# Optimization experiments

Hardware: AMD Instinct MI355X
Metric: run time of the kernel (lower is better)

The kernel has to match this reference:

```python
import jax, jax.numpy as jnp
import numpy as np

D_MODEL = 1024
N_HEADS = 16


def setup_inputs() -> dict:
    key0 = jax.random.key(0)
    ks = jax.random.split(key0, 13)
    B, Lq, Lk, D = 2, 1024, 2048, D_MODEL
    scale = 0.02
    inp = {
        "query": jax.random.normal(ks[0], (B, Lq, D), jnp.float32),
        "key": jax.random.normal(ks[1], (B, Lk, D), jnp.float32),
        "value": jax.random.normal(ks[2], (B, Lk, D), jnp.float32),
        "mask": jax.random.randint(ks[3], (B, 1, Lq, Lk), 0, 2, jnp.int32),
        "attn_bias": jax.random.normal(ks[4], (B, N_HEADS, Lq, Lk), jnp.float32) * 0.1,
        "Wq": jax.random.normal(ks[5], (D, D), jnp.float32) * scale,
        "bq": jnp.zeros((D,), jnp.float32),
        "Wk": jax.random.normal(ks[6], (D, D), jnp.float32) * scale,
        "bk": jnp.zeros((D,), jnp.float32),
        "Wv": jax.random.normal(ks[7], (D, D), jnp.float32) * scale,
        "bv": jnp.zeros((D,), jnp.float32),
        "Wo": jax.random.normal(ks[8], (D, D), jnp.float32) * scale,
        "bo": jnp.zeros((D,), jnp.float32),
    }
    return inp


def reference(query, key, value, mask, attn_bias, Wq, bq, Wk, bk, Wv, bv, Wo, bo):
    B, Lq, D = query.shape
    Lk = key.shape[1]
    H = N_HEADS
    dh = D // H
    # projections (torch Linear: x @ W.T + b), then split heads -> [B,H,L,dh]
    Q = (query @ Wq.T + bq).reshape(B, Lq, H, dh).transpose(0, 2, 1, 3)
    K = (key @ Wk.T + bk).reshape(B, Lk, H, dh).transpose(0, 2, 1, 3)
    V = (value @ Wv.T + bv).reshape(B, Lk, H, dh).transpose(0, 2, 1, 3)
    scores = jnp.einsum("bhqd,bhkd->bhqk", Q, K) / jnp.sqrt(jnp.float32(dh))
    scores = scores + attn_bias
    scores = jnp.where(mask == 0, jnp.float32(-1e9), scores)
    attn = jax.nn.softmax(scores, axis=-1)  # dropout disabled (eval / p=0)
    out = jnp.einsum("bhqk,bhkd->bhqd", attn, V)
    out = out.transpose(0, 2, 1, 3).reshape(B, Lq, D)
    out = out @ Wo.T + bo
    return out, attn
```

## Files before the change

kernel.cpp:

```cpp
#include <hip/hip_runtime.h>
#include <hip/hip_bf16.h>

typedef __hip_bfloat16 bf16;
typedef __bf16  bf16x8 __attribute__((ext_vector_type(8)));
typedef float   f32x4  __attribute__((ext_vector_type(4)));

static constexpr int DMODEL = 1024;
static constexpr int NHEADS = 16;
static constexpr int DHEAD  = 64;
static constexpr int BATCH  = 2;
static constexpr int SLQ    = 1024;
static constexpr int SLK    = 2048;
static constexpr size_t OUTQ = (size_t)BATCH * SLQ * DMODEL;

__global__ __launch_bounds__(256)
void k_cvt(const float* __restrict__ q,  const float* __restrict__ k,
           const float* __restrict__ v,  const float* __restrict__ wq,
           const float* __restrict__ wk, const float* __restrict__ wv,
           const float* __restrict__ wo,
           bf16* __restrict__ qb,  bf16* __restrict__ kb,  bf16* __restrict__ vb,
           bf16* __restrict__ wqb, bf16* __restrict__ wkb, bf16* __restrict__ wvb,
           bf16* __restrict__ wob)
{
    const int seg = blockIdx.y;
    const float* s; bf16* d; int n;
    switch (seg) {
        case 0:  s = q;  d = qb;  n = 2 * 1024 * 1024; break;
        case 1:  s = k;  d = kb;  n = 4 * 1024 * 1024; break;
        case 2:  s = v;  d = vb;  n = 4 * 1024 * 1024; break;
        case 3:  s = wq; d = wqb; n = 1024 * 1024; break;
        case 4:  s = wk; d = wkb; n = 1024 * 1024; break;
        case 5:  s = wv; d = wvb; n = 1024 * 1024; break;
        default: s = wo; d = wob; n = 1024 * 1024; break;
    }
    const int stride = gridDim.x * blockDim.x;
    for (int i = blockIdx.x * blockDim.x + threadIdx.x; i * 8 < n; i += stride) {
        const float4 a = *(const float4*)(s + (size_t)i * 8);
        const float4 b = *(const float4*)(s + (size_t)i * 8 + 4);
        bf16 h[8] = {__float2bfloat16(a.x), __float2bfloat16(a.y),
                     __float2bfloat16(a.z), __float2bfloat16(a.w),
                     __float2bfloat16(b.x), __float2bfloat16(b.y),
                     __float2bfloat16(b.z), __float2bfloat16(b.w)};
        *(int4*)(d + (size_t)i * 8) = *(const int4*)h;
    }
}

__device__ __forceinline__ void gemm128(const bf16* __restrict__ A,
                                        const bf16* __restrict__ W,
                                        int m0, int n0, f32x4 acc[4][4])
{
    __shared__ __align__(16) unsigned short As[128][40];
    __shared__ __align__(16) unsigned short Bs[128][40];
    const int tid  = threadIdx.x;
    const int lane = tid & 63, w = tid >> 6;
    const int wr = (w >> 1) * 64, wc = (w & 1) * 64;
    const int lr = lane & 15, lk = lane >> 4;
    const int srow = tid >> 1;
    const int scol = (tid & 1) * 16;

    const bf16* Ap = A + (size_t)(m0 + srow) * DMODEL + scol;
    const bf16* Wp = W + (size_t)(n0 + srow) * DMODEL + scol;

    for (int kt = 0; kt < DMODEL; kt += 32) {
        *(int4*)&As[srow][scol]     = *(const int4*)(Ap + kt);
        *(int4*)&As[srow][scol + 8] = *(const int4*)(Ap + kt + 8);
        *(int4*)&Bs[srow][scol]     = *(const int4*)(Wp + kt);
        *(int4*)&Bs[srow][scol + 8] = *(const int4*)(Wp + kt + 8);
        __syncthreads();
        bf16x8 av[4], wv[4];
#pragma unroll
        for (int i = 0; i < 4; ++i)
            av[i] = *(const bf16x8*)&As[wr + i * 16 + lr][lk * 8];
#pragma unroll
        for (int j = 0; j < 4; ++j)
            wv[j] = *(const bf16x8*)&Bs[wc + j * 16 + lr][lk * 8];
#pragma unroll
        for (int i = 0; i < 4; ++i)
#pragma unroll
            for (int j = 0; j < 4; ++j)
                acc[i][j] = __builtin_amdgcn_mfma_f32_16x16x32_bf16(av[i], wv[j], acc[i][j], 0, 0, 0);
        __syncthreads();
    }
}

__global__ __launch_bounds__(256)
void k_qkv(const bf16* __restrict__ qb, const bf16* __restrict__ kb,
           const bf16* __restrict__ vb2,
           const bf16* __restrict__ wqb, const bf16* __restrict__ wkb,
           const bf16* __restrict__ wvb,
           const float* __restrict__ bq, const float* __restrict__ bk,
           const float* __restrict__ bvv,
           bf16* __restrict__ Qp, bf16* __restrict__ Kp, bf16* __restrict__ Vt)
{
    const int which = blockIdx.z;
    const int m0 = blockIdx.x * 128, n0 = blockIdx.y * 128;
    if (which == 0 && m0 >= BATCH * SLQ) return;
    const bf16* A = which == 0 ? qb : which == 1 ? kb : vb2;
    const bf16* W = which == 0 ? wqb : which == 1 ? wkb : wvb;
    const float* bias = which == 0 ? bq : which == 1 ? bk : bvv;

    f32x4 acc[4][4] = {};
    gemm128(A, W, m0, n0, acc);

    const int tid = threadIdx.x, lane = tid & 63, w = tid >> 6;
    const int wr = (w >> 1) * 64, wc = (w & 1) * 64;
    const int lr = lane & 15, lk = lane >> 4;

    if (which < 2) {
        bf16* C = which == 0 ? Qp : Kp;
#pragma unroll
        for (int i = 0; i < 4; ++i)
#pragma unroll
            for (int j = 0; j < 4; ++j) {
                const int col = n0 + wc + j * 16 + lr;
                const float bvx = bias[col];
#pragma unroll
                for (int r = 0; r < 4; ++r) {
                    const int row = m0 + wr + i * 16 + lk * 4 + r;
                    C[(size_t)row * DMODEL + col] = __float2bfloat16(acc[i][j][r] + bvx);
                }
            }
    } else {
#pragma unroll
        for (int i = 0; i < 4; ++i)
#pragma unroll
            for (int j = 0; j < 4; ++j) {
                const int col = n0 + wc + j * 16 + lr;
                const float bvx = bias[col];
                const int h = col >> 6, d = col & 63;
                const int mb = m0 + wr + i * 16 + lk * 4;
                const int b = mb >> 11, kk = mb & 2047;
                bf16* dst = Vt + ((size_t)(b * NHEADS + h) * DHEAD + d) * SLK + kk;
#pragma unroll
                for (int r = 0; r < 4; ++r)
                    dst[r] = __float2bfloat16(acc[i][j][r] + bvx);
            }
    }
}

__global__ __launch_bounds__(256)
void k_projO(const bf16* __restrict__ ctx, const bf16* __restrict__ wob,
             const float* __restrict__ bo, float* __restrict__ out)
{
    const int m0 = blockIdx.x * 128, n0 = blockIdx.y * 128;
    f32x4 acc[4][4] = {};
    gemm128(ctx, wob, m0, n0, acc);
    const int tid = threadIdx.x, lane = tid & 63, w = tid >> 6;
    const int wr = (w >> 1) * 64, wc = (w & 1) * 64;
    const int lr = lane & 15, lk = lane >> 4;
#pragma unroll
    for (int i = 0; i < 4; ++i)
#pragma unroll
        for (int j = 0; j < 4; ++j) {
            const int col = n0 + wc + j * 16 + lr;
            const float bvx = bo[col];
#pragma unroll
            for (int r = 0; r < 4; ++r) {
                const int row = m0 + wr + i * 16 + lk * 4 + r;
                out[(size_t)row * DMODEL + col] = acc[i][j][r] + bvx;
            }
        }
}

__global__ __launch_bounds__(1024, 4)
void k_attn(const bf16* __restrict__ Qp, const bf16* __restrict__ Kp,
            const float* __restrict__ bias, const int* __restrict__ mask,
            const bf16* __restrict__ Vt, float* __restrict__ attn,
            bf16* __restrict__ ctx)
{
    constexpr int SST = 2052;
    constexpr int PST = 520;

    __shared__ __align__(16) float S[16 * SST];
    __shared__ __align__(16) bf16  Pc[16 * PST];
    __shared__ float m_s[16], inv_s[16];

    const int qt = blockIdx.x, bh = blockIdx.y;
    const int b = bh >> 4, h = bh & 15;
    const int q0 = qt * 16;
    const int tid  = threadIdx.x;
    const int lane = tid & 63, w = tid >> 6;
    const int lr = lane & 15, lk = lane >> 4;

    const bf16* qb = Qp + ((size_t)(b * SLQ + q0 + lr)) * DMODEL + h * DHEAD + lk * 8;
    const bf16x8 a0 = *(const bf16x8*)qb;
    const bf16x8 a1 = *(const bf16x8*)(qb + 32);

    const bf16* kb = Kp + (size_t)b * SLK * DMODEL + h * DHEAD + lk * 8;
#pragma unroll 2
    for (int ct = 0; ct < 8; ++ct) {
        const int c0 = w * 128 + ct * 16;
        const bf16* kp = kb + (size_t)(c0 + lr) * DMODEL;
        bf16x8 b0 = *(const bf16x8*)kp;
        bf16x8 b1 = *(const bf16x8*)(kp + 32);
        f32x4 acc = {0.f, 0.f, 0.f, 0.f};
        acc = __builtin_amdgcn_mfma_f32_16x16x32_bf16(a0, b0, acc, 0, 0, 0);
        acc = __builtin_amdgcn_mfma_f32_16x16x32_bf16(a1, b1, acc, 0, 0, 0);
#pragma unroll
        for (int r = 0; r < 4; ++r)
            S[(lk * 4 + r) * SST + c0 + lr] = acc[r] * 0.125f;
    }
    __syncthreads();

    {
        float* sp = &S[w * SST];
        const size_t brow = ((size_t)bh * SLQ + q0 + w) * SLK;
        const size_t mrow = ((size_t)b  * SLQ + q0 + w) * SLK;
        float mx = -3.0e38f;
#pragma unroll 2
        for (int j = 0; j < 8; ++j) {
            const int col = j * 256 + lane * 4;
            f32x4 v = *(const f32x4*)(sp + col);
            const float4 bb = *(const float4*)(bias + brow + col);
            const int4  mm = *(const int4*)(mask + mrow + col);
            float s0 = (mm.x == 0) ? -1e9f : v[0] + bb.x;
            float s1 = (mm.y == 0) ? -1e9f : v[1] + bb.y;
            float s2 = (mm.z == 0) ? -1e9f : v[2] + bb.z;
            float s3 = (mm.w == 0) ? -1e9f : v[3] + bb.w;
            f32x4 wv = {s0, s1, s2, s3};
            *(f32x4*)(sp + col) = wv;
            mx = fmaxf(mx, fmaxf(fmaxf(s0, s1), fmaxf(s2, s3)));
        }
#pragma unroll
        for (int d = 1; d < 64; d <<= 1) mx = fmaxf(mx, __shfl_xor(mx, d));
        float l = 0.f;
#pragma unroll 2
        for (int j = 0; j < 8; ++j) {
            const int col = j * 256 + lane * 4;
            const f32x4 v = *(const f32x4*)(sp + col);
            l += __expf(v[0] - mx) + __expf(v[1] - mx)
               + __expf(v[2] - mx) + __expf(v[3] - mx);
        }
#pragma unroll
        for (int d = 1; d < 64; d <<= 1) l += __shfl_xor(l, d);
        if (lane == 0) { m_s[w] = mx; inv_s[w] = 1.0f / l; }
    }
    __syncthreads();

    f32x4 pv = {0.f, 0.f, 0.f, 0.f};
    const int g = w >> 2, dg = w & 3;
    const bf16* vb = Vt + (size_t)bh * DHEAD * SLK + (size_t)(dg * 16 + lr) * SLK + lk * 8;
    for (int c = 0; c < 4; ++c) {
        const int ck0 = c * 512;
        {
            const int scol = lane * 8;
            const float m = m_s[w], inv = inv_s[w];
            const f32x4 s0 = *(const f32x4*)&S[w * SST + ck0 + scol];
            const f32x4 s1 = *(const f32x4*)&S[w * SST + ck0 + scol + 4];
            const f32x4 p0 = {__expf(s0[0] - m) * inv, __expf(s0[1] - m) * inv,
                              __expf(s0[2] - m) * inv, __expf(s0[3] - m) * inv};
            const f32x4 p1 = {__expf(s1[0] - m) * inv, __expf(s1[1] - m) * inv,
                              __expf(s1[2] - m) * inv, __expf(s1[3] - m) * inv};
            float* ap = attn + ((size_t)bh * SLQ + q0 + w) * SLK + ck0 + scol;
            __builtin_nontemporal_store(p0, (f32x4*)ap);
            __builtin_nontemporal_store(p1, (f32x4*)(ap + 4));
            bf16 t8[8] = {__float2bfloat16(p0[0]), __float2bfloat16(p0[1]),
                          __float2bfloat16(p0[2]), __float2bfloat16(p0[3]),
                          __float2bfloat16(p1[0]), __float2bfloat16(p1[1]),
                          __float2bfloat16(p1[2]), __float2bfloat16(p1[3])};
            *(int4*)&Pc[w * PST + scol] = *(const int4*)t8;
        }
        __syncthreads();
        const bf16* vc = vb + ck0;
#pragma unroll
        for (int i = 0; i < 4; ++i) {
            const int koff = (g * 4 + i) * 32;
            bf16x8 pa = *(const bf16x8*)&Pc[lr * PST + koff + lk * 8];
            bf16x8 vv = *(const bf16x8*)(vc + koff);
            pv = __builtin_amdgcn_mfma_f32_16x16x32_bf16(pa, vv, pv, 0, 0, 0);
        }
        __syncthreads();
    }

    float* rbuf = S;
    *(f32x4*)&rbuf[(w * 64 + lane) * 4] = pv;
    __syncthreads();
    if (g == 0) {
        f32x4 t = {0.f, 0.f, 0.f, 0.f};
#pragma unroll
        for (int gg = 0; gg < 4; ++gg)
            t += *(const f32x4*)&rbuf[((gg * 4 + dg) * 64 + lane) * 4];
        const int d = dg * 16 + lr;
#pragma unroll
        for (int r = 0; r < 4; ++r) {
            const int q = lk * 4 + r;
            ctx[((size_t)(b * SLQ + q0 + q)) * DMODEL + h * DHEAD + d] =
                __float2bfloat16(t[r]);
        }
    }
}

extern "C" void kernel_launch(void* const* d_in, const int* in_sizes, int n_in,
                              void* d_out, int out_size, void* d_ws, size_t ws_size,
                              hipStream_t stream)
{
    const float* query = (const float*)d_in[0];
    const float* key   = (const float*)d_in[1];
    const float* value = (const float*)d_in[2];
    const int*   mask  = (const int*)d_in[3];
    const float* bias  = (const float*)d_in[4];
    const float* Wq = (const float*)d_in[5];
    const float* bq = (const float*)d_in[6];
    const float* Wk = (const float*)d_in[7];
    const float* bk = (const float*)d_in[8];
    const float* Wv = (const float*)d_in[9];
    const float* bv = (const float*)d_in[10];
    const float* Wo = (const float*)d_in[11];
    const float* bo = (const float*)d_in[12];

    float* out  = (float*)d_out;
    float* attn = out + OUTQ;

    bf16* Qp  = (bf16*)d_ws;
    bf16* ctx = Qp;
    bf16* Wob = Qp + (size_t)2 * 1024 * 1024;
    bf16* Vt  = Qp + (size_t)4 * 1024 * 1024;
    bf16* Kp  = (bf16*)d_out;

    bf16* qbf = (bf16*)attn;
    bf16* kbf = qbf + (size_t)2 * 1024 * 1024;
    bf16* vbf = kbf + (size_t)4 * 1024 * 1024;
    bf16* Wqb = vbf + (size_t)4 * 1024 * 1024;
    bf16* Wkb = Wqb + (size_t)1024 * 1024;
    bf16* Wvb = Wkb + (size_t)1024 * 1024;

    k_cvt<<<dim3(256, 7), dim3(256), 0, stream>>>(query, key, value, Wq, Wk, Wv, Wo,
                                                  qbf, kbf, vbf, Wqb, Wkb, Wvb, Wob);
    k_qkv<<<dim3(32, 8, 3), dim3(256), 0, stream>>>(qbf, kbf, vbf, Wqb, Wkb, Wvb,
                                                    bq, bk, bv, Qp, Kp, Vt);
    k_attn<<<dim3(SLQ / 16, BATCH * NHEADS), dim3(1024), 0, stream>>>(Qp, Kp, bias, mask, Vt, attn, ctx);
    k_projO<<<dim3(16, 8), dim3(256), 0, stream>>>(ctx, Wob, bo, out);
}
```

Measured before the change: 708.2 us.

## Use direct global-to-LDS loads in GEMM and prefetch bias/mask in attention

The GEMM tile loader now uses global_load_lds, moving data straight from global memory into unpadded LDS tiles instead of staging it through registers. Separately, the attention kernel issues its bias and mask loads for the first 16 rows at kernel start, before the QK^T MFMA, so their latency overlaps the score computation. The unpadded LDS layout (row stride 32) can cause bank conflicts on the MFMA fragment reads. The prefetch holds 64 extra VGPRs per thread, which may lower occupancy.

```diff
diff --git a/kernel.cpp b/kernel.cpp
--- a/kernel.cpp
+++ b/kernel.cpp
@@ -12,6 +12,10 @@
 static constexpr int SLQ    = 1024;
 static constexpr int SLK    = 2048;
 static constexpr size_t OUTQ = (size_t)BATCH * SLQ * DMODEL;
+
+#define GLOAD16(g, l) __builtin_amdgcn_global_load_lds(                        \
+    (const __attribute__((address_space(1))) unsigned int*)(g),                \
+    (__attribute__((address_space(3))) unsigned int*)(l), 16, 0, 0)
 
 __global__ __launch_bounds__(256)
 void k_cvt(const float* __restrict__ q,  const float* __restrict__ k,
@@ -49,31 +53,39 @@
                                         const bf16* __restrict__ W,
                                         int m0, int n0, f32x4 acc[4][4])
 {
-    __shared__ __align__(16) unsigned short As[128][40];
-    __shared__ __align__(16) unsigned short Bs[128][40];
+    __shared__ __align__(16) unsigned short As[128 * 32];
+    __shared__ __align__(16) unsigned short Bs[128 * 32];
     const int tid  = threadIdx.x;
     const int lane = tid & 63, w = tid >> 6;
     const int wr = (w >> 1) * 64, wc = (w & 1) * 64;
     const int lr = lane & 15, lk = lane >> 4;
-    const int srow = tid >> 1;
-    const int scol = (tid & 1) * 16;
-
-    const bf16* Ap = A + (size_t)(m0 + srow) * DMODEL + scol;
-    const bf16* Wp = W + (size_t)(n0 + srow) * DMODEL + scol;
+
+    const int seg0 = w * 2, seg1 = w * 2 + 1;
+    const int r0 = seg0 * 16 + (lane >> 2);
+    const int r1 = seg1 * 16 + (lane >> 2);
+    const int ce = (lane & 3) * 8;
+    const bf16* a0p = A + (size_t)(m0 + r0) * DMODEL + ce;
+    const bf16* a1p = A + (size_t)(m0 + r1) * DMODEL + ce;
+    const bf16* w0p = W + (size_t)(n0 + r0) * DMODEL + ce;
+    const bf16* w1p = W + (size_t)(n0 + r1) * DMODEL + ce;
+    unsigned short* as0 = &As[seg0 * 512];
+    unsigned short* as1 = &As[seg1 * 512];
+    unsigned short* bs0 = &Bs[seg0 * 512];
+    unsigned short* bs1 = &Bs[seg1 * 512];
 
     for (int kt = 0; kt < DMODEL; kt += 32) {
-        *(int4*)&As[srow][scol]     = *(const int4*)(Ap + kt);
-        *(int4*)&As[srow][scol + 8] = *(const int4*)(Ap + kt + 8);
-        *(int4*)&Bs[srow][scol]     = *(const int4*)(Wp + kt);
-        *(int4*)&Bs[srow][scol + 8] = *(const int4*)(Wp + kt + 8);
+        GLOAD16(a0p + kt, as0);
+        GLOAD16(a1p + kt, as1);
+        GLOAD16(w0p + kt, bs0);
+        GLOAD16(w1p + kt, bs1);
         __syncthreads();
         bf16x8 av[4], wv[4];
 #pragma unroll
         for (int i = 0; i < 4; ++i)
-            av[i] = *(const bf16x8*)&As[wr + i * 16 + lr][lk * 8];
+            av[i] = *(const bf16x8*)&As[(wr + i * 16 + lr) * 32 + lk * 8];
 #pragma unroll
         for (int j = 0; j < 4; ++j)
-            wv[j] = *(const bf16x8*)&Bs[wc + j * 16 + lr][lk * 8];
+            wv[j] = *(const bf16x8*)&Bs[(wc + j * 16 + lr) * 32 + lk * 8];
 #pragma unroll
         for (int i = 0; i < 4; ++i)
 #pragma unroll
@@ -181,6 +193,17 @@
     const int tid  = threadIdx.x;
     const int lane = tid & 63, w = tid >> 6;
     const int lr = lane & 15, lk = lane >> 4;
+
+    f32x4 bb[8]; int4 mm[8];
+    {
+        const size_t brow = ((size_t)bh * SLQ + q0 + w) * SLK;
+        const size_t mrow = ((size_t)b  * SLQ + q0 + w) * SLK;
+#pragma unroll
+        for (int j = 0; j < 8; ++j) {
+            bb[j] = *(const f32x4*)(bias + brow + j * 256 + lane * 4);
+            mm[j] = *(const int4*)(mask + mrow + j * 256 + lane * 4);
+        }
+    }
 
     const bf16* qb = Qp + ((size_t)(b * SLQ + q0 + lr)) * DMODEL + h * DHEAD + lk * 8;
     const bf16x8 a0 = *(const bf16x8*)qb;
@@ -204,19 +227,15 @@
 
     {
         float* sp = &S[w * SST];
-        const size_t brow = ((size_t)bh * SLQ + q0 + w) * SLK;
-        const size_t mrow = ((size_t)b  * SLQ + q0 + w) * SLK;
         float mx = -3.0e38f;
-#pragma unroll 2
+#pragma unroll
         for (int j = 0; j < 8; ++j) {
             const int col = j * 256 + lane * 4;
             f32x4 v = *(const f32x4*)(sp + col);
-            const float4 bb = *(const float4*)(bias + brow + col);
-            const int4  mm = *(const int4*)(mask + mrow + col);
-            float s0 = (mm.x == 0) ? -1e9f : v[0] + bb.x;
-            float s1 = (mm.y == 0) ? -1e9f : v[1] + bb.y;
-            float s2 = (mm.z == 0) ? -1e9f : v[2] + bb.z;
-            float s3 = (mm.w == 0) ? -1e9f : v[3] + bb.w;
+            float s0 = (mm[j].x == 0) ? -1e9f : v[0] + bb[j][0];
+            float s1 = (mm[j].y == 0) ? -1e9f : v[1] + bb[j][1];
+            float s2 = (mm[j].z == 0) ? -1e9f : v[2] + bb[j][2];
+            float s3 = (mm[j].w == 0) ? -1e9f : v[3] + bb[j][3];
             f32x4 wv = {s0, s1, s2, s3};
             *(f32x4*)(sp + col) = wv;
             mx = fmaxf(mx, fmaxf(fmaxf(s0, s1), fmaxf(s2, s3)));
```

Result: no change. 699.0 us (-1.3%).
